# Optimization experiments

Measured on AMD Instinct MI355X. Metric: run time of the kernel, lower is better.

Reference implementation:

```python
import jax, jax.numpy as jnp
import numpy as np

N_NODES = 50000
N_EDGES = 800000
IN_CH, HID, OUT_CH, EDGE_DIM = 256, 128, 64, 64
NUM_LAYERS = 3


def _linear_init(key, fan_in, fan_out):
    # torch nn.Linear default: U(-1/sqrt(fan_in), 1/sqrt(fan_in))
    kw, kb = jax.random.split(key)
    bound = 1.0 / np.sqrt(fan_in)
    W = jax.random.uniform(kw, (fan_in, fan_out), minval=-bound, maxval=bound, dtype=jnp.float32)
    b = jax.random.uniform(kb, (fan_out,), minval=-bound, maxval=bound, dtype=jnp.float32)
    return W, b


def setup_inputs() -> dict:
    key = jax.random.key(0)
    ks = jax.random.split(key, 8)
    x = jax.random.normal(ks[0], (N_NODES, IN_CH), dtype=jnp.float32)
    edge_index = jax.random.randint(ks[1], (2, N_EDGES), 0, N_NODES, dtype=jnp.int64)
    edge_attr = jax.random.normal(ks[2], (N_EDGES, EDGE_DIM), dtype=jnp.float32)
    W_in, b_in = _linear_init(ks[3], IN_CH, HID)
    W_e, b_e = _linear_init(ks[4], EDGE_DIM, HID)
    W1, b1 = _linear_init(ks[5], HID, HID)
    W2, b2 = _linear_init(ks[6], HID, HID)
    W_out, b_out = _linear_init(ks[7], HID, OUT_CH)
    return {"x": x, "edge_index": edge_index, "edge_attr": edge_attr,
            "W_in": W_in, "b_in": b_in, "W_e": W_e, "b_e": b_e,
            "W1": W1, "b1": b1, "W2": W2, "b2": b2,
            "W_out": W_out, "b_out": b_out}


def reference(x, edge_index, edge_attr, W_in, b_in, W_e, b_e, W1, b1, W2, b2, W_out, b_out):
    N = x.shape[0]
    src, dst = edge_index[0], edge_index[1]
    # input projection (in_channels != hidden_channels)
    h = x @ W_in + b_in                      # [N, HID]
    # edge projection is layer-independent (shared GINEConv weights)
    e = edge_attr @ W_e + b_e                # [E, HID]
    for _ in range(NUM_LAYERS):
        # GINEConv: message = relu(h_src + e), sum-aggregate to dst, eps=0
        msg = jax.nn.relu(h[src] + e)        # [E, HID]
        agg = jax.ops.segment_sum(msg, dst, num_segments=N)
        z = h + agg                          # (1+eps)*h + agg, eps=0
        # conv nn: MLP Linear->relu->Linear (plain_last)
        z = jax.nn.relu(z @ W1 + b1) @ W2 + b2
        # outer act
        h = jax.nn.relu(z)
    return h @ W_out + b_out                 # [N, OUT_CH]
```

## Files before the change

### kernel.cpp

```cpp
#include <hip/hip_runtime.h>
#include <hip/hip_bf16.h>
#include <stdint.h>

#define N_NODES 50000
#define N_EDGES 800000
#define IN_CH 256
#define HID 128
#define OUT_CH 64
#define EDGE_DIM 64

typedef __hip_bfloat16 bf16;
typedef __attribute__((ext_vector_type(8))) short short8;
typedef __attribute__((ext_vector_type(4))) float f32x4;

__device__ __forceinline__ void st_out(float* p, float v) { *p = v; }
__device__ __forceinline__ void st_out(bf16* p, float v) { *p = __float2bfloat16(v); }

__device__ __forceinline__ void wt_one(const float* W, bf16* Wt, int K, int N, int i) {
    int n = i % N, k = i / N;
    Wt[n * K + k] = __float2bfloat16(W[i]);
}
__launch_bounds__(256)
__global__ void wt_prep_all(const float* W_in, const float* W_e, const float* W1,
                            const float* W2, const float* W_out,
                            bf16* Wt_in, bf16* Wt_e, bf16* Wt_1, bf16* Wt_2, bf16* Wt_out) {
    int i = blockIdx.x * 256 + threadIdx.x;
    if (i < 32768)       wt_one(W_in,  Wt_in,  256, 128, i);
    else if (i < 40960)  wt_one(W_e,   Wt_e,    64, 128, i - 32768);
    else if (i < 57344)  wt_one(W1,    Wt_1,   128, 128, i - 40960);
    else if (i < 73728)  wt_one(W2,    Wt_2,   128, 128, i - 57344);
    else if (i < 81920)  wt_one(W_out, Wt_out, 128,  64, i - 73728);
}

template<int KTOT, int N, int MROWS, bool RELU, bool PERM, typename InT, typename OutT>
__launch_bounds__(256)
__global__ void gemm_mfma(const InT* __restrict__ A, const bf16* __restrict__ Wt,
                          const float* __restrict__ b, OutT* __restrict__ out,
                          int M, const int* __restrict__ operm) {
    static_assert(KTOT % 64 == 0, "");
    constexpr int KC  = 64;
    constexpr int NCH = KTOT / KC;
    constexpr int KCP = KC + 8;
    constexpr int NT  = N / 16;
    constexpr int MT  = MROWS / 64;
    __shared__ __align__(16) bf16 Ws[N * KCP];
    __shared__ __align__(16) bf16 As[MROWS * KCP];

    const int tid  = threadIdx.x;
    const int wave = tid >> 6;
    const int lane = tid & 63;
    const int quad = lane >> 4;
    const int l16  = lane & 15;
    const int base = blockIdx.x * MROWS;

    f32x4 acc[MT][NT];
    #pragma unroll
    for (int m = 0; m < MT; m++)
        #pragma unroll
        for (int i = 0; i < NT; i++) acc[m][i] = (f32x4){0.f, 0.f, 0.f, 0.f};

    for (int ch = 0; ch < NCH; ch++) {
        const int kc = ch * KC;
        constexpr int WIT = N * KC / (256 * 8);
        #pragma unroll
        for (int it = 0; it < WIT; it++) {
            int t8 = (it * 256 + tid) * 8;
            int n = t8 / KC, k = t8 % KC;
            *(uint4*)&Ws[n * KCP + k] = *(const uint4*)&Wt[n * KTOT + kc + k];
        }
        if constexpr (sizeof(InT) == 4) {
            constexpr int AIT = MROWS * KC / (256 * 4);
            #pragma unroll
            for (int it = 0; it < AIT; it++) {
                int t4 = (it * 256 + tid) * 4;
                int r = t4 / KC, k = t4 % KC;
                int gr = base + r;
                float4 v = (gr < M) ? *(const float4*)&A[(size_t)gr * KTOT + kc + k]
                                    : make_float4(0.f, 0.f, 0.f, 0.f);
                *(__hip_bfloat162*)&As[r * KCP + k]     = __float22bfloat162_rn(make_float2(v.x, v.y));
                *(__hip_bfloat162*)&As[r * KCP + k + 2] = __float22bfloat162_rn(make_float2(v.z, v.w));
            }
        } else {
            constexpr int AIT = MROWS * KC / (256 * 8);
            #pragma unroll
            for (int it = 0; it < AIT; it++) {
                int t8 = (it * 256 + tid) * 8;
                int r = t8 / KC, k = t8 % KC;
                int gr = base + r;
                uint4 v = (gr < M) ? *(const uint4*)&A[(size_t)gr * KTOT + kc + k]
                                   : make_uint4(0u, 0u, 0u, 0u);
                *(uint4*)&As[r * KCP + k] = v;
            }
        }
        __syncthreads();

        #pragma unroll
        for (int ks = 0; ks < KC / 32; ks++) {
            short8 af[MT];
            #pragma unroll
            for (int m = 0; m < MT; m++)
                af[m] = *(const short8*)&As[(wave * MT * 16 + m * 16 + l16) * KCP + ks * 32 + quad * 8];
            #pragma unroll
            for (int nt = 0; nt < NT; nt++) {
                short8 bfr = *(const short8*)&Ws[(nt * 16 + l16) * KCP + ks * 32 + quad * 8];
                #pragma unroll
                for (int m = 0; m < MT; m++)
                    acc[m][nt] = __builtin_amdgcn_mfma_f32_16x16x32_bf16(af[m], bfr, acc[m][nt], 0, 0, 0);
            }
        }
        __syncthreads();
    }

    #pragma unroll
    for (int m = 0; m < MT; m++) {
        const int r0 = base + wave * MT * 16 + m * 16 + quad * 4;
        #pragma unroll
        for (int reg = 0; reg < 4; reg++) {
            int gr = r0 + reg;
            if (gr < M) {
                int orow = PERM ? operm[gr] : gr;
                #pragma unroll
                for (int nt = 0; nt < NT; nt++) {
                    int col = nt * 16 + l16;
                    float v = acc[m][nt][reg] + b[col];
                    if (RELU) v = fmaxf(v, 0.f);
                    st_out(&out[(size_t)orow * N + col], v);
                }
            }
        }
    }
}

__launch_bounds__(256)
__global__ void hist_kernel(const int* __restrict__ ei, int* __restrict__ counts) {
    int edge = blockIdx.x * 256 + threadIdx.x;
    if (edge < N_EDGES) atomicAdd(&counts[ei[N_EDGES + edge]], 1);
}

__launch_bounds__(1024)
__global__ void scan_kernel(const int* __restrict__ counts, int* __restrict__ offsets,
                            int* __restrict__ cursor) {
    __shared__ int part[1024];
    const int tid = threadIdx.x;
    const int CH = (N_NODES + 1023) / 1024;
    int beg = tid * CH, end = min(beg + CH, N_NODES);
    int s = 0;
    for (int i = beg; i < end; i++) s += counts[i];
    part[tid] = s;
    __syncthreads();
    for (int off = 1; off < 1024; off <<= 1) {
        int t = (tid >= off) ? part[tid - off] : 0;
        __syncthreads();
        part[tid] += t;
        __syncthreads();
    }
    int run = (tid == 0) ? 0 : part[tid - 1];
    for (int i = beg; i < end; i++) {
        offsets[i] = run;
        cursor[i] = run;
        run += counts[i];
    }
    if (tid == 1023) offsets[N_NODES] = part[1023];
}

__launch_bounds__(256)
__global__ void scatter_perm(const int* __restrict__ ei, int* __restrict__ cursor,
                             int* __restrict__ pos_of_edge, int* __restrict__ src_sorted) {
    int edge = blockIdx.x * 256 + threadIdx.x;
    if (edge >= N_EDGES) return;
    int dst = ei[N_EDGES + edge];
    int pos = atomicAdd(&cursor[dst], 1);
    pos_of_edge[edge] = pos;
    src_sorted[pos] = ei[edge];
}

__device__ __forceinline__ float blo(uint32_t u) { return __uint_as_float(u << 16); }
__device__ __forceinline__ float bhi(uint32_t u) { return __uint_as_float(u & 0xffff0000u); }

__launch_bounds__(256)
__global__ void agg_kernel(const int* __restrict__ offsets, const int* __restrict__ src_sorted,
                           const bf16* __restrict__ e, const bf16* __restrict__ h,
                           bf16* __restrict__ z) {
    int wid = (blockIdx.x * 256 + threadIdx.x) >> 6;
    int lane = threadIdx.x & 63;
    if (wid >= N_NODES) return;
    int beg = offsets[wid], end = offsets[wid + 1];
    int c = lane * 2;
    float2 acc = {0.f, 0.f};
    int i = beg;
    for (; i + 1 < end; i += 2) {
        int s0 = src_sorted[i], s1 = src_sorted[i + 1];
        uint32_t ev0 = *(const uint32_t*)&e[i * HID + c];
        uint32_t ev1 = *(const uint32_t*)&e[(i + 1) * HID + c];
        uint32_t h0 = *(const uint32_t*)&h[s0 * HID + c];
        uint32_t h1 = *(const uint32_t*)&h[s1 * HID + c];
        acc.x += fmaxf(blo(h0) + blo(ev0), 0.f);
        acc.y += fmaxf(bhi(h0) + bhi(ev0), 0.f);
        acc.x += fmaxf(blo(h1) + blo(ev1), 0.f);
        acc.y += fmaxf(bhi(h1) + bhi(ev1), 0.f);
    }
    if (i < end) {
        int s0 = src_sorted[i];
        uint32_t ev0 = *(const uint32_t*)&e[i * HID + c];
        uint32_t h0 = *(const uint32_t*)&h[s0 * HID + c];
        acc.x += fmaxf(blo(h0) + blo(ev0), 0.f);
        acc.y += fmaxf(bhi(h0) + bhi(ev0), 0.f);
    }
    uint32_t hs = *(const uint32_t*)&h[wid * HID + c];
    acc.x += blo(hs);
    acc.y += bhi(hs);
    __hip_bfloat162 p = __float22bfloat162_rn(make_float2(acc.x, acc.y));
    *(__hip_bfloat162*)&z[wid * HID + c] = p;
}

extern "C" void kernel_launch(void* const* d_in, const int* in_sizes, int n_in,
                              void* d_out, int out_size, void* d_ws, size_t ws_size,
                              hipStream_t stream) {
    const float* x     = (const float*)d_in[0];
    const int*   ei    = (const int*)d_in[1];
    const float* ea    = (const float*)d_in[2];
    const float* W_in  = (const float*)d_in[3];
    const float* b_in  = (const float*)d_in[4];
    const float* W_e   = (const float*)d_in[5];
    const float* b_e   = (const float*)d_in[6];
    const float* W1    = (const float*)d_in[7];
    const float* b1    = (const float*)d_in[8];
    const float* W2    = (const float*)d_in[9];
    const float* b2    = (const float*)d_in[10];
    const float* W_out = (const float*)d_in[11];
    const float* b_out = (const float*)d_in[12];
    float* out = (float*)d_out;

    char* ws = (char*)d_ws;
    size_t off = 0;
    bf16*  h       = (bf16*) (ws + off); off += (size_t)N_NODES * HID * 2;
    bf16*  z       = (bf16*) (ws + off); off += (size_t)N_NODES * HID * 2;
    bf16*  e       = (bf16*) (ws + off); off += (size_t)N_EDGES * HID * 2;
    int*   counts  = (int*)  (ws + off); off += (size_t)N_NODES * 4;
    int*   offsets = (int*)  (ws + off); off += (size_t)(N_NODES + 1) * 4;
    int*   cursor  = (int*)  (ws + off); off += (size_t)N_NODES * 4;
    int*   poe     = (int*)  (ws + off); off += (size_t)N_EDGES * 4;
    int*   srcs    = (int*)  (ws + off); off += (size_t)N_EDGES * 4;
    bf16*  Wt_in   = (bf16*) (ws + off); off += (size_t)HID * IN_CH * 2;
    bf16*  Wt_e    = (bf16*) (ws + off); off += (size_t)HID * EDGE_DIM * 2;
    bf16*  Wt_1    = (bf16*) (ws + off); off += (size_t)HID * HID * 2;
    bf16*  Wt_2    = (bf16*) (ws + off); off += (size_t)HID * HID * 2;
    bf16*  Wt_out  = (bf16*) (ws + off); off += (size_t)OUT_CH * HID * 2;

    wt_prep_all<<<(81920 + 255) / 256, 256, 0, stream>>>(
        W_in, W_e, W1, W2, W_out, Wt_in, Wt_e, Wt_1, Wt_2, Wt_out);

    hipMemsetAsync(counts, 0, (size_t)N_NODES * 4, stream);
    hist_kernel<<<(N_EDGES + 255) / 256, 256, 0, stream>>>(ei, counts);
    scan_kernel<<<1, 1024, 0, stream>>>(counts, offsets, cursor);
    scatter_perm<<<(N_EDGES + 255) / 256, 256, 0, stream>>>(ei, cursor, poe, srcs);

    gemm_mfma<IN_CH, HID, 64, false, false, float, bf16>
        <<<(N_NODES + 63) / 64, 256, 0, stream>>>(x, Wt_in, b_in, h, N_NODES, nullptr);

    gemm_mfma<EDGE_DIM, HID, 128, false, true, float, bf16>
        <<<(N_EDGES + 127) / 128, 256, 0, stream>>>(ea, Wt_e, b_e, e, N_EDGES, poe);

    for (int layer = 0; layer < 3; ++layer) {
        agg_kernel<<<(N_NODES * 64 + 255) / 256, 256, 0, stream>>>(offsets, srcs, e, h, z);
        gemm_mfma<HID, HID, 64, true, false, bf16, bf16>
            <<<(N_NODES + 63) / 64, 256, 0, stream>>>(z, Wt_1, b1, h, N_NODES, nullptr);
        gemm_mfma<HID, HID, 64, true, false, bf16, bf16>
            <<<(N_NODES + 63) / 64, 256, 0, stream>>>(h, Wt_2, b2, z, N_NODES, nullptr);
        bf16* t = h; h = z; z = t;
    }

    gemm_mfma<HID, OUT_CH, 64, false, false, bf16, float>
        <<<(N_NODES + 63) / 64, 256, 0, stream>>>(h, Wt_out, b_out, out, N_NODES, nullptr);
}
```

Measured before the change: 888.5 us.

## Gather edge rows on GEMM input and vectorize aggregation with 16-byte loads

The edge-projection GEMM now gathers input rows through a sorted-edge index and writes its output contiguously, where it previously scattered output rows through a permutation. The aggregation kernel is restructured so each wave processes four edges at once. Each 16-lane group loads 16-byte chunks, and source indices are fetched cooperatively once per 64 edges and broadcast with shuffles. Partial sums are then reduced across groups with xor shuffles. This aims for wider, more coalesced loads and more memory-level parallelism in the gather-heavy aggregation, at the cost of shuffle reductions and idle lanes on low-degree nodes.

```diff
diff --git a/kernel.cpp b/kernel.cpp
--- a/kernel.cpp
+++ b/kernel.cpp
@@ -32,11 +32,11 @@
     else if (i < 81920)  wt_one(W_out, Wt_out, 128,  64, i - 73728);
 }
 
-template<int KTOT, int N, int MROWS, bool RELU, bool PERM, typename InT, typename OutT>
+template<int KTOT, int N, int MROWS, bool RELU, bool GATHER, typename InT, typename OutT>
 __launch_bounds__(256)
 __global__ void gemm_mfma(const InT* __restrict__ A, const bf16* __restrict__ Wt,
                           const float* __restrict__ b, OutT* __restrict__ out,
-                          int M, const int* __restrict__ operm) {
+                          int M, const int* __restrict__ gidx) {
     static_assert(KTOT % 64 == 0, "");
     constexpr int KC  = 64;
     constexpr int NCH = KTOT / KC;
@@ -75,8 +75,11 @@
                 int t4 = (it * 256 + tid) * 4;
                 int r = t4 / KC, k = t4 % KC;
                 int gr = base + r;
-                float4 v = (gr < M) ? *(const float4*)&A[(size_t)gr * KTOT + kc + k]
-                                    : make_float4(0.f, 0.f, 0.f, 0.f);
+                float4 v = make_float4(0.f, 0.f, 0.f, 0.f);
+                if (gr < M) {
+                    int ar = GATHER ? gidx[gr] : gr;
+                    v = *(const float4*)&A[(size_t)ar * KTOT + kc + k];
+                }
                 *(__hip_bfloat162*)&As[r * KCP + k]     = __float22bfloat162_rn(make_float2(v.x, v.y));
                 *(__hip_bfloat162*)&As[r * KCP + k + 2] = __float22bfloat162_rn(make_float2(v.z, v.w));
             }
@@ -87,8 +90,11 @@
                 int t8 = (it * 256 + tid) * 8;
                 int r = t8 / KC, k = t8 % KC;
                 int gr = base + r;
-                uint4 v = (gr < M) ? *(const uint4*)&A[(size_t)gr * KTOT + kc + k]
-                                   : make_uint4(0u, 0u, 0u, 0u);
+                uint4 v = make_uint4(0u, 0u, 0u, 0u);
+                if (gr < M) {
+                    int ar = GATHER ? gidx[gr] : gr;
+                    v = *(const uint4*)&A[(size_t)ar * KTOT + kc + k];
+                }
                 *(uint4*)&As[r * KCP + k] = v;
             }
         }
@@ -118,13 +124,12 @@
         for (int reg = 0; reg < 4; reg++) {
             int gr = r0 + reg;
             if (gr < M) {
-                int orow = PERM ? operm[gr] : gr;
                 #pragma unroll
                 for (int nt = 0; nt < NT; nt++) {
                     int col = nt * 16 + l16;
                     float v = acc[m][nt][reg] + b[col];
                     if (RELU) v = fmaxf(v, 0.f);
-                    st_out(&out[(size_t)orow * N + col], v);
+                    st_out(&out[(size_t)gr * N + col], v);
                 }
             }
         }
@@ -165,12 +170,12 @@
 
 __launch_bounds__(256)
 __global__ void scatter_perm(const int* __restrict__ ei, int* __restrict__ cursor,
-                             int* __restrict__ pos_of_edge, int* __restrict__ src_sorted) {
+                             int* __restrict__ esort, int* __restrict__ src_sorted) {
     int edge = blockIdx.x * 256 + threadIdx.x;
     if (edge >= N_EDGES) return;
     int dst = ei[N_EDGES + edge];
     int pos = atomicAdd(&cursor[dst], 1);
-    pos_of_edge[edge] = pos;
+    esort[pos] = edge;
     src_sorted[pos] = ei[edge];
 }
 
@@ -184,33 +189,54 @@
     int wid = (blockIdx.x * 256 + threadIdx.x) >> 6;
     int lane = threadIdx.x & 63;
     if (wid >= N_NODES) return;
-    int beg = offsets[wid], end = offsets[wid + 1];
-    int c = lane * 2;
-    float2 acc = {0.f, 0.f};
-    int i = beg;
-    for (; i + 1 < end; i += 2) {
-        int s0 = src_sorted[i], s1 = src_sorted[i + 1];
-        uint32_t ev0 = *(const uint32_t*)&e[i * HID + c];
-        uint32_t ev1 = *(const uint32_t*)&e[(i + 1) * HID + c];
-        uint32_t h0 = *(const uint32_t*)&h[s0 * HID + c];
-        uint32_t h1 = *(const uint32_t*)&h[s1 * HID + c];
-        acc.x += fmaxf(blo(h0) + blo(ev0), 0.f);
-        acc.y += fmaxf(bhi(h0) + bhi(ev0), 0.f);
-        acc.x += fmaxf(blo(h1) + blo(ev1), 0.f);
-        acc.y += fmaxf(bhi(h1) + bhi(ev1), 0.f);
-    }
-    if (i < end) {
-        int s0 = src_sorted[i];
-        uint32_t ev0 = *(const uint32_t*)&e[i * HID + c];
-        uint32_t h0 = *(const uint32_t*)&h[s0 * HID + c];
-        acc.x += fmaxf(blo(h0) + blo(ev0), 0.f);
-        acc.y += fmaxf(bhi(h0) + bhi(ev0), 0.f);
-    }
-    uint32_t hs = *(const uint32_t*)&h[wid * HID + c];
-    acc.x += blo(hs);
-    acc.y += bhi(hs);
-    __hip_bfloat162 p = __float22bfloat162_rn(make_float2(acc.x, acc.y));
-    *(__hip_bfloat162*)&z[wid * HID + c] = p;
+    const int beg = offsets[wid], end = offsets[wid + 1];
+    const int q   = lane >> 4;
+    const int l16 = lane & 15;
+    const int c8  = l16 * 8;
+
+    float acc[8];
+    #pragma unroll
+    for (int j = 0; j < 8; j++) acc[j] = 0.f;
+
+    for (int w = beg; w < end; w += 64) {
+        const int cnt = min(64, end - w);
+        int my_src = (w + lane < end) ? src_sorted[w + lane] : 0;
+        for (int i = 0; i < cnt; i += 4) {
+            bool ok = (i + q) < cnt;
+            int s = __shfl(my_src, (i + q) & 63);
+            uint4 ev = make_uint4(0u, 0u, 0u, 0u);
+            uint4 hv = make_uint4(0u, 0u, 0u, 0u);
+            if (ok) {
+                ev = *(const uint4*)&e[(size_t)(w + i) * HID + lane * 8];
+                hv = *(const uint4*)&h[(size_t)s * HID + c8];
+            }
+            uint32_t evs[4] = {ev.x, ev.y, ev.z, ev.w};
+            uint32_t hvs[4] = {hv.x, hv.y, hv.z, hv.w};
+            #pragma unroll
+            for (int j = 0; j < 4; j++) {
+                acc[2 * j]     += fmaxf(blo(evs[j]) + blo(hvs[j]), 0.f);
+                acc[2 * j + 1] += fmaxf(bhi(evs[j]) + bhi(hvs[j]), 0.f);
+            }
+        }
+    }
+    #pragma unroll
+    for (int j = 0; j < 8; j++) {
+        acc[j] += __shfl_xor(acc[j], 16);
+        acc[j] += __shfl_xor(acc[j], 32);
+    }
+    if (lane < 16) {
+        uint4 hs = *(const uint4*)&h[(size_t)wid * HID + c8];
+        uint32_t hss[4] = {hs.x, hs.y, hs.z, hs.w};
+        uint32_t o[4];
+        #pragma unroll
+        for (int j = 0; j < 4; j++) {
+            float lo = acc[2 * j]     + blo(hss[j]);
+            float hi = acc[2 * j + 1] + bhi(hss[j]);
+            __hip_bfloat162 p = __float22bfloat162_rn(make_float2(lo, hi));
+            o[j] = *(uint32_t*)&p;
+        }
+        *(uint4*)&z[(size_t)wid * HID + c8] = make_uint4(o[0], o[1], o[2], o[3]);
+    }
 }
 
 extern "C" void kernel_launch(void* const* d_in, const int* in_sizes, int n_in,
@@ -239,7 +265,7 @@
     int*   counts  = (int*)  (ws + off); off += (size_t)N_NODES * 4;
     int*   offsets = (int*)  (ws + off); off += (size_t)(N_NODES + 1) * 4;
     int*   cursor  = (int*)  (ws + off); off += (size_t)N_NODES * 4;
-    int*   poe     = (int*)  (ws + off); off += (size_t)N_EDGES * 4;
+    int*   esort   = (int*)  (ws + off); off += (size_t)N_EDGES * 4;
     int*   srcs    = (int*)  (ws + off); off += (size_t)N_EDGES * 4;
     bf16*  Wt_in   = (bf16*) (ws + off); off += (size_t)HID * IN_CH * 2;
     bf16*  Wt_e    = (bf16*) (ws + off); off += (size_t)HID * EDGE_DIM * 2;
@@ -253,13 +279,13 @@
     hipMemsetAsync(counts, 0, (size_t)N_NODES * 4, stream);
     hist_kernel<<<(N_EDGES + 255) / 256, 256, 0, stream>>>(ei, counts);
     scan_kernel<<<1, 1024, 0, stream>>>(counts, offsets, cursor);
-    scatter_perm<<<(N_EDGES + 255) / 256, 256, 0, stream>>>(ei, cursor, poe, srcs);
+    scatter_perm<<<(N_EDGES + 255) / 256, 256, 0, stream>>>(ei, cursor, esort, srcs);
 
     gemm_mfma<IN_CH, HID, 64, false, false, float, bf16>
         <<<(N_NODES + 63) / 64, 256, 0, stream>>>(x, Wt_in, b_in, h, N_NODES, nullptr);
 
     gemm_mfma<EDGE_DIM, HID, 128, false, true, float, bf16>
-        <<<(N_EDGES + 127) / 128, 256, 0, stream>>>(ea, Wt_e, b_e, e, N_EDGES, poe);
+        <<<(N_EDGES + 127) / 128, 256, 0, stream>>>(ea, Wt_e, b_e, e, N_EDGES, esort);
 
     for (int layer = 0; layer < 3; ++layer) {
         agg_kernel<<<(N_NODES * 64 + 255) / 256, 256, 0, stream>>>(offsets, srcs, e, h, z);
```

Result: no change. 899.0 us (+1.2%).

## Recompute edge projection inside aggregation from a permuted bf16 edge_attr

Applied to the files above, without the earlier changes.

The edge projection is no longer stored as an [E,128] bf16 tensor. edge_attr is instead permuted into dst-sorted order as bf16 [E,64], and each layer's aggregation kernel recomputes the projection with MFMA into shared memory. Blocks are assigned edge chunks through a new blkstart table built in the scan kernel, and each block gathers h for the nodes whose edges start in its chunk. This halves the edge-feature traffic read on every layer, at the cost of repeated small GEMMs and possible load imbalance. Edges per block are capped at 128, so graphs with very high-degree nodes could be truncated.

```diff
diff --git a/kernel.cpp b/kernel.cpp
--- a/kernel.cpp
+++ b/kernel.cpp
@@ -8,6 +8,10 @@
 #define HID 128
 #define OUT_CH 64
 #define EDGE_DIM 64
+
+#define AGG_EW  64
+#define AGG_CAP 128
+#define AGG_B   (N_EDGES / AGG_EW)
 
 typedef __hip_bfloat16 bf16;
 typedef __attribute__((ext_vector_type(8))) short short8;
@@ -32,11 +36,10 @@
     else if (i < 81920)  wt_one(W_out, Wt_out, 128,  64, i - 73728);
 }
 
-template<int KTOT, int N, int MROWS, bool RELU, bool PERM, typename InT, typename OutT>
+template<int KTOT, int N, int MROWS, bool RELU, typename InT, typename OutT>
 __launch_bounds__(256)
 __global__ void gemm_mfma(const InT* __restrict__ A, const bf16* __restrict__ Wt,
-                          const float* __restrict__ b, OutT* __restrict__ out,
-                          int M, const int* __restrict__ operm) {
+                          const float* __restrict__ b, OutT* __restrict__ out, int M) {
     static_assert(KTOT % 64 == 0, "");
     constexpr int KC  = 64;
     constexpr int NCH = KTOT / KC;
@@ -118,13 +121,12 @@
         for (int reg = 0; reg < 4; reg++) {
             int gr = r0 + reg;
             if (gr < M) {
-                int orow = PERM ? operm[gr] : gr;
                 #pragma unroll
                 for (int nt = 0; nt < NT; nt++) {
                     int col = nt * 16 + l16;
                     float v = acc[m][nt][reg] + b[col];
                     if (RELU) v = fmaxf(v, 0.f);
-                    st_out(&out[(size_t)orow * N + col], v);
+                    st_out(&out[(size_t)gr * N + col], v);
                 }
             }
         }
@@ -139,7 +141,7 @@
 
 __launch_bounds__(1024)
 __global__ void scan_kernel(const int* __restrict__ counts, int* __restrict__ offsets,
-                            int* __restrict__ cursor) {
+                            int* __restrict__ cursor, int* __restrict__ blkstart) {
     __shared__ int part[1024];
     const int tid = threadIdx.x;
     const int CH = (N_NODES + 1023) / 1024;
@@ -161,56 +163,140 @@
         run += counts[i];
     }
     if (tid == 1023) offsets[N_NODES] = part[1023];
+    __syncthreads();
+    int vp = (beg == 0) ? -1 : offsets[beg - 1];
+    for (int n = beg; n < end; n++) {
+        int v = offsets[n];
+        int blo_ = (vp < 0) ? 0 : (vp / AGG_EW + 1);
+        int bhi_ = v / AGG_EW;
+        for (int bb = blo_; bb <= bhi_; bb++) blkstart[bb] = n;
+        vp = v;
+    }
+    if (tid == 1023) {
+        int vpN = offsets[N_NODES - 1];
+        int blo_ = vpN / AGG_EW + 1;
+        for (int bb = blo_; bb <= AGG_B; bb++) blkstart[bb] = N_NODES;
+        blkstart[AGG_B + 1] = N_NODES;
+    }
 }
 
 __launch_bounds__(256)
 __global__ void scatter_perm(const int* __restrict__ ei, int* __restrict__ cursor,
-                             int* __restrict__ pos_of_edge, int* __restrict__ src_sorted) {
+                             int* __restrict__ poe, int* __restrict__ srcs) {
     int edge = blockIdx.x * 256 + threadIdx.x;
     if (edge >= N_EDGES) return;
     int dst = ei[N_EDGES + edge];
     int pos = atomicAdd(&cursor[dst], 1);
-    pos_of_edge[edge] = pos;
-    src_sorted[pos] = ei[edge];
+    poe[edge] = pos;
+    srcs[pos] = ei[edge];
+}
+
+__launch_bounds__(256)
+__global__ void ea_permute(const float* __restrict__ ea, const int* __restrict__ poe,
+                           bf16* __restrict__ eas) {
+    int t = blockIdx.x * 256 + threadIdx.x;
+    int edge = t >> 4, l16 = t & 15;
+    if (edge >= N_EDGES) return;
+    float4 v = *(const float4*)&ea[(size_t)edge * EDGE_DIM + l16 * 4];
+    int pos = poe[edge];
+    __hip_bfloat162 p0 = __float22bfloat162_rn(make_float2(v.x, v.y));
+    __hip_bfloat162 p1 = __float22bfloat162_rn(make_float2(v.z, v.w));
+    uint2 u = make_uint2(*(uint32_t*)&p0, *(uint32_t*)&p1);
+    *(uint2*)&eas[(size_t)pos * EDGE_DIM + l16 * 4] = u;
 }
 
 __device__ __forceinline__ float blo(uint32_t u) { return __uint_as_float(u << 16); }
 __device__ __forceinline__ float bhi(uint32_t u) { return __uint_as_float(u & 0xffff0000u); }
 
 __launch_bounds__(256)
-__global__ void agg_kernel(const int* __restrict__ offsets, const int* __restrict__ src_sorted,
-                           const bf16* __restrict__ e, const bf16* __restrict__ h,
-                           bf16* __restrict__ z) {
-    int wid = (blockIdx.x * 256 + threadIdx.x) >> 6;
-    int lane = threadIdx.x & 63;
-    if (wid >= N_NODES) return;
-    int beg = offsets[wid], end = offsets[wid + 1];
-    int c = lane * 2;
-    float2 acc = {0.f, 0.f};
-    int i = beg;
-    for (; i + 1 < end; i += 2) {
-        int s0 = src_sorted[i], s1 = src_sorted[i + 1];
-        uint32_t ev0 = *(const uint32_t*)&e[i * HID + c];
-        uint32_t ev1 = *(const uint32_t*)&e[(i + 1) * HID + c];
-        uint32_t h0 = *(const uint32_t*)&h[s0 * HID + c];
-        uint32_t h1 = *(const uint32_t*)&h[s1 * HID + c];
-        acc.x += fmaxf(blo(h0) + blo(ev0), 0.f);
-        acc.y += fmaxf(bhi(h0) + bhi(ev0), 0.f);
-        acc.x += fmaxf(blo(h1) + blo(ev1), 0.f);
-        acc.y += fmaxf(bhi(h1) + bhi(ev1), 0.f);
-    }
-    if (i < end) {
-        int s0 = src_sorted[i];
-        uint32_t ev0 = *(const uint32_t*)&e[i * HID + c];
-        uint32_t h0 = *(const uint32_t*)&h[s0 * HID + c];
-        acc.x += fmaxf(blo(h0) + blo(ev0), 0.f);
-        acc.y += fmaxf(bhi(h0) + bhi(ev0), 0.f);
-    }
-    uint32_t hs = *(const uint32_t*)&h[wid * HID + c];
-    acc.x += blo(hs);
-    acc.y += bhi(hs);
-    __hip_bfloat162 p = __float22bfloat162_rn(make_float2(acc.x, acc.y));
-    *(__hip_bfloat162*)&z[wid * HID + c] = p;
+__global__ void agg_fused(const int* __restrict__ offsets, const int* __restrict__ blkstart,
+                          const int* __restrict__ srcs, const bf16* __restrict__ eas,
+                          const bf16* __restrict__ Wt_e, const float* __restrict__ b_e,
+                          const bf16* __restrict__ h, bf16* __restrict__ z) {
+    constexpr int P = 136;
+    __shared__ __align__(16) bf16 et[AGG_CAP * P];
+    __shared__ int srcs_s[AGG_CAP];
+
+    const int b    = blockIdx.x;
+    const int tid  = threadIdx.x;
+    const int wave = tid >> 6;
+    const int lane = tid & 63;
+    const int quad = lane >> 4;
+    const int l16  = lane & 15;
+
+    const int n0 = blkstart[b], n1 = blkstart[b + 1];
+    if (n0 >= n1) return;
+    const int e0 = offsets[n0];
+    int e1 = offsets[n1];
+    if (e1 > e0 + AGG_CAP) e1 = e0 + AGG_CAP;
+    const int ne = e1 - e0;
+
+    if (tid < AGG_CAP) srcs_s[tid] = (tid < ne) ? srcs[e0 + tid] : 0;
+
+    short8 af[2][2];
+    float4 bias[2];
+    #pragma unroll
+    for (int ct = 0; ct < 2; ct++) {
+        int chr = (wave * 2 + ct) * 16 + l16;
+        #pragma unroll
+        for (int ks = 0; ks < 2; ks++)
+            af[ct][ks] = *(const short8*)&Wt_e[chr * EDGE_DIM + ks * 32 + quad * 8];
+        bias[ct] = *(const float4*)&b_e[(wave * 2 + ct) * 16 + quad * 4];
+    }
+    const int nsub = (ne + 15) >> 4;
+    for (int es = 0; es < nsub; es++) {
+        int erow = es * 16 + l16;
+        int ge = e0 + erow;
+        short8 bf0 = (short8){0,0,0,0,0,0,0,0}, bf1 = bf0;
+        if (erow < ne) {
+            bf0 = *(const short8*)&eas[(size_t)ge * EDGE_DIM + quad * 8];
+            bf1 = *(const short8*)&eas[(size_t)ge * EDGE_DIM + 32 + quad * 8];
+        }
+        #pragma unroll
+        for (int ct = 0; ct < 2; ct++) {
+            f32x4 acc = (f32x4){0.f, 0.f, 0.f, 0.f};
+            acc = __builtin_amdgcn_mfma_f32_16x16x32_bf16(af[ct][0], bf0, acc, 0, 0, 0);
+            acc = __builtin_amdgcn_mfma_f32_16x16x32_bf16(af[ct][1], bf1, acc, 0, 0, 0);
+            int row = es * 16 + l16;
+            int ch0 = (wave * 2 + ct) * 16 + quad * 4;
+            __hip_bfloat162 p0 = __float22bfloat162_rn(make_float2(acc[0] + bias[ct].x, acc[1] + bias[ct].y));
+            __hip_bfloat162 p1 = __float22bfloat162_rn(make_float2(acc[2] + bias[ct].z, acc[3] + bias[ct].w));
+            *(uint2*)&et[row * P + ch0] = make_uint2(*(uint32_t*)&p0, *(uint32_t*)&p1);
+        }
+    }
+    __syncthreads();
+
+    const int c = lane * 2;
+    for (int n = n0 + wave; n < n1; n += 4) {
+        int s  = offsets[n] - e0;
+        int ee = offsets[n + 1] - e0;
+        if (ee > ne) ee = ne;
+        float2 a = make_float2(0.f, 0.f);
+        int i = s;
+        for (; i + 1 < ee; i += 2) {
+            int s0 = srcs_s[i], s1 = srcs_s[i + 1];
+            uint32_t ev0 = *(const uint32_t*)&et[i * P + c];
+            uint32_t ev1 = *(const uint32_t*)&et[(i + 1) * P + c];
+            uint32_t h0 = *(const uint32_t*)&h[(size_t)s0 * HID + c];
+            uint32_t h1 = *(const uint32_t*)&h[(size_t)s1 * HID + c];
+            a.x += fmaxf(blo(h0) + blo(ev0), 0.f);
+            a.y += fmaxf(bhi(h0) + bhi(ev0), 0.f);
+            a.x += fmaxf(blo(h1) + blo(ev1), 0.f);
+            a.y += fmaxf(bhi(h1) + bhi(ev1), 0.f);
+        }
+        if (i < ee) {
+            int s0 = srcs_s[i];
+            uint32_t ev0 = *(const uint32_t*)&et[i * P + c];
+            uint32_t h0 = *(const uint32_t*)&h[(size_t)s0 * HID + c];
+            a.x += fmaxf(blo(h0) + blo(ev0), 0.f);
+            a.y += fmaxf(bhi(h0) + bhi(ev0), 0.f);
+        }
+        uint32_t hn = *(const uint32_t*)&h[(size_t)n * HID + c];
+        a.x += blo(hn);
+        a.y += bhi(hn);
+        __hip_bfloat162 p = __float22bfloat162_rn(make_float2(a.x, a.y));
+        *(uint32_t*)&z[(size_t)n * HID + c] = *(uint32_t*)&p;
+    }
 }
 
 extern "C" void kernel_launch(void* const* d_in, const int* in_sizes, int n_in,
@@ -233,43 +319,43 @@
 
     char* ws = (char*)d_ws;
     size_t off = 0;
-    bf16*  h       = (bf16*) (ws + off); off += (size_t)N_NODES * HID * 2;
-    bf16*  z       = (bf16*) (ws + off); off += (size_t)N_NODES * HID * 2;
-    bf16*  e       = (bf16*) (ws + off); off += (size_t)N_EDGES * HID * 2;
-    int*   counts  = (int*)  (ws + off); off += (size_t)N_NODES * 4;
-    int*   offsets = (int*)  (ws + off); off += (size_t)(N_NODES + 1) * 4;
-    int*   cursor  = (int*)  (ws + off); off += (size_t)N_NODES * 4;
-    int*   poe     = (int*)  (ws + off); off += (size_t)N_EDGES * 4;
-    int*   srcs    = (int*)  (ws + off); off += (size_t)N_EDGES * 4;
-    bf16*  Wt_in   = (bf16*) (ws + off); off += (size_t)HID * IN_CH * 2;
-    bf16*  Wt_e    = (bf16*) (ws + off); off += (size_t)HID * EDGE_DIM * 2;
-    bf16*  Wt_1    = (bf16*) (ws + off); off += (size_t)HID * HID * 2;
-    bf16*  Wt_2    = (bf16*) (ws + off); off += (size_t)HID * HID * 2;
-    bf16*  Wt_out  = (bf16*) (ws + off); off += (size_t)OUT_CH * HID * 2;
+    bf16*  h        = (bf16*) (ws + off); off += (size_t)N_NODES * HID * 2;
+    bf16*  z        = (bf16*) (ws + off); off += (size_t)N_NODES * HID * 2;
+    bf16*  eas      = (bf16*) (ws + off); off += (size_t)N_EDGES * EDGE_DIM * 2;
+    int*   counts   = (int*)  (ws + off); off += (size_t)N_NODES * 4;
+    int*   offsets  = (int*)  (ws + off); off += (size_t)(N_NODES + 1) * 4;
+    int*   cursor   = (int*)  (ws + off); off += (size_t)N_NODES * 4;
+    int*   poe      = (int*)  (ws + off); off += (size_t)N_EDGES * 4;
+    int*   srcs     = (int*)  (ws + off); off += (size_t)N_EDGES * 4;
+    int*   blkstart = (int*)  (ws + off); off += (size_t)(AGG_B + 2) * 4;
+    bf16*  Wt_in    = (bf16*) (ws + off); off += (size_t)HID * IN_CH * 2;
+    bf16*  Wt_e     = (bf16*) (ws + off); off += (size_t)HID * EDGE_DIM * 2;
+    bf16*  Wt_1     = (bf16*) (ws + off); off += (size_t)HID * HID * 2;
+    bf16*  Wt_2     = (bf16*) (ws + off); off += (size_t)HID * HID * 2;
+    bf16*  Wt_out   = (bf16*) (ws + off); off += (size_t)OUT_CH * HID * 2;
 
     wt_prep_all<<<(81920 + 255) / 256, 256, 0, stream>>>(
         W_in, W_e, W1, W2, W_out, Wt_in, Wt_e, Wt_1, Wt_2, Wt_out);
 
     hipMemsetAsync(counts, 0, (size_t)N_NODES * 4, stream);
     hist_kernel<<<(N_EDGES + 255) / 256, 256, 0, stream>>>(ei, counts);
-    scan_kernel<<<1, 1024, 0, stream>>>(counts, offsets, cursor);
+    scan_kernel<<<1, 1024, 0, stream>>>(counts, offsets, cursor, blkstart);
     scatter_perm<<<(N_EDGES + 255) / 256, 256, 0, stream>>>(ei, cursor, poe, srcs);
 
-    gemm_mfma<IN_CH, HID, 64, false, false, float, bf16>
-        <<<(N_NODES + 63) / 64, 256, 0, stream>>>(x, Wt_in, b_in, h, N_NODES, nullptr);
-
-    gemm_mfma<EDGE_DIM, HID, 128, false, true, float, bf16>
-        <<<(N_EDGES + 127) / 128, 256, 0, stream>>>(ea, Wt_e, b_e, e, N_EDGES, poe);
+    ea_permute<<<(N_EDGES * 16 + 255) / 256, 256, 0, stream>>>(ea, poe, eas);
+
+    gemm_mfma<IN_CH, HID, 64, false, float, bf16>
+        <<<(N_NODES + 63) / 64, 256, 0, stream>>>(x, Wt_in, b_in, h, N_NODES);
 
     for (int layer = 0; layer < 3; ++layer) {
-        agg_kernel<<<(N_NODES * 64 + 255) / 256, 256, 0, stream>>>(offsets, srcs, e, h, z);
-        gemm_mfma<HID, HID, 64, true, false, bf16, bf16>
-            <<<(N_NODES + 63) / 64, 256, 0, stream>>>(z, Wt_1, b1, h, N_NODES, nullptr);
-        gemm_mfma<HID, HID, 64, true, false, bf16, bf16>
-            <<<(N_NODES + 63) / 64, 256, 0, stream>>>(h, Wt_2, b2, z, N_NODES, nullptr);
+        agg_fused<<<AGG_B + 1, 256, 0, stream>>>(offsets, blkstart, srcs, eas, Wt_e, b_e, h, z);
+        gemm_mfma<HID, HID, 64, true, bf16, bf16>
+            <<<(N_NODES + 63) / 64, 256, 0, stream>>>(z, Wt_1, b1, h, N_NODES);
+        gemm_mfma<HID, HID, 64, true, bf16, bf16>
+            <<<(N_NODES + 63) / 64, 256, 0, stream>>>(h, Wt_2, b2, z, N_NODES);
         bf16* t = h; h = z; z = t;
     }
 
-    gemm_mfma<HID, OUT_CH, 64, false, false, bf16, float>
-        <<<(N_NODES + 63) / 64, 256, 0, stream>>>(h, Wt_out, b_out, out, N_NODES, nullptr);
-}
+    gemm_mfma<HID, OUT_CH, 64, false, bf16, float>
+        <<<(N_NODES + 63) / 64, 256, 0, stream>>>(h, Wt_out, b_out, out, N_NODES);
+}
```

After: 1.096 ms. +23.4%, slower.
